# Kernel tuning notes

Hardware: AMD Instinct MI355X
Metric: run time of the kernel (lower is better)

## Reference

```python
import jax, jax.numpy as jnp
import numpy as np

DIM = 768

def setup_inputs() -> dict:
    key = jax.random.key(0)
    ks = jax.random.split(key, 11)
    B, N = 4, 2048
    s = 1.0 / np.sqrt(DIM)
    inp = {
        "q": jax.random.normal(ks[0], (B, N, DIM), jnp.float32),
        "k": jax.random.normal(ks[1], (B, N, DIM), jnp.float32),
        "v": jax.random.normal(ks[2], (B, N, DIM), jnp.float32),
        "Wq": jax.random.normal(ks[3], (DIM, DIM), jnp.float32) * s,
        "bq": jnp.zeros((DIM,), jnp.float32),
        "Wk": jax.random.normal(ks[4], (DIM, DIM), jnp.float32) * s,
        "bk": jnp.zeros((DIM,), jnp.float32),
        "Wv": jax.random.normal(ks[5], (DIM, DIM), jnp.float32) * s,
        "bv": jnp.zeros((DIM,), jnp.float32),
        "Wp": jax.random.normal(ks[6], (DIM, DIM), jnp.float32) * s,
        "bp": jnp.zeros((DIM,), jnp.float32),
    }
    return inp

def reference(q, k, v, Wq, bq, Wk, bk, Wv, bv, Wp, bp):
    # Linear projections (torch Linear: x @ W.T + b)
    scale = DIM ** (-0.5)  # note: full dim, num_heads unused in original forward
    qp = q @ Wq.T + bq            # [B, Nq, D]
    kp = k @ Wk.T + bk            # [B, Nk, D]
    vp = v @ Wv.T + bv            # [B, Nk, D]
    attn = jnp.einsum('bqd,bkd->bqk', qp * scale, kp)  # [B, Nq, Nk]
    attn = jax.nn.softmax(attn, axis=-1)
    x = jnp.einsum('bqk,bkd->bqd', attn, vp)           # [B, Nq, D]
    return x @ Wp.T + bp
```

## Files before the change

### kernel.cpp

```cpp
#include <hip/hip_runtime.h>
#include <hip/hip_bf16.h>
#include <math.h>

typedef __bf16 bf16x8 __attribute__((ext_vector_type(8)));
typedef float  f32x4  __attribute__((ext_vector_type(4)));
typedef float  f32x4v __attribute__((ext_vector_type(4)));
typedef unsigned short ushort_t;
typedef ushort_t u16x4 __attribute__((ext_vector_type(4)));
typedef ushort_t u16x8 __attribute__((ext_vector_type(8)));

__device__ __forceinline__ ushort_t f2bf(float f) {
    unsigned u = __builtin_bit_cast(unsigned, f);
    u += 0x7FFFu + ((u >> 16) & 1u);
    return (ushort_t)(u >> 16);
}
__device__ __forceinline__ float bf2f(ushort_t b) {
    return __builtin_bit_cast(float, (unsigned)b << 16);
}

__device__ __forceinline__ void xcd_remap(int& bx, int& by, int& bz) {
    const int gx = gridDim.x, gy = gridDim.y;
    const int nwg = gx * gy * gridDim.z;
    const int lin = (blockIdx.z * gy + blockIdx.y) * gx + blockIdx.x;
    const int chunk = nwg >> 3;
    int nid = (lin & 7) * chunk + (lin >> 3);
    bx = nid % gx; nid /= gx;
    by = nid % gy; bz = nid / gy;
}

__global__ __launch_bounds__(256)
void cvt_all(const float* __restrict__ v, const float* __restrict__ Wq,
             const float* __restrict__ Wk, const float* __restrict__ Wv,
             const float* __restrict__ Wp,
             ushort_t* __restrict__ vb, ushort_t* __restrict__ Wqb,
             ushort_t* __restrict__ Wkb, ushort_t* __restrict__ Wvb,
             ushort_t* __restrict__ Wpb, float* __restrict__ rowsum)
{
    const int b = blockIdx.x;
    if (b < 6144) {
        int i = b * 256 + threadIdx.x;
        f32x4v x = ((const f32x4v*)v)[i];
        u16x4 o = { f2bf(x.x), f2bf(x.y), f2bf(x.z), f2bf(x.w) };
        ((u16x4*)vb)[i] = o;
    } else if (b < 8448) {
        const int w = (b - 6144) / 576;
        const int bb = (b - 6144) % 576;
        const float* in  = w == 0 ? Wq : w == 1 ? Wk : w == 2 ? Wv : Wp;
        ushort_t*    out = w == 0 ? Wqb : w == 1 ? Wkb : w == 2 ? Wvb : Wpb;
        int i = bb * 256 + threadIdx.x;
        f32x4v x = ((const f32x4v*)in)[i];
        u16x4 o = { f2bf(x.x), f2bf(x.y), f2bf(x.z), f2bf(x.w) };
        ((u16x4*)out)[i] = o;
    } else {
        int i = (b - 8448) * 256 + threadIdx.x;
        rowsum[i] = 0.f;
    }
}

#define GEMM256_CORE(Ab_, lda_, Bb_, ldb_, Kdim_)                                           \
    __shared__ __align__(16) ushort_t lds[2][2][2][128 * 64];                               \
    const int tid  = threadIdx.x;                                                           \
    const int lane = tid & 63;                                                              \
    const int wave = tid >> 6;                                                              \
    const int wm = wave >> 2, wn = wave & 3;                                                \
    const int r16 = lane & 15, kb = lane >> 4;                                              \
    f32x4 acc[8][4];                                                                        \
    _Pragma("unroll") for (int i = 0; i < 8; ++i)                                           \
        _Pragma("unroll") for (int j = 0; j < 4; ++j)                                       \
            acc[i][j] = (f32x4){0.f, 0.f, 0.f, 0.f};                                        \
    auto stage = [&](int kt) {                                                              \
        const int d  = kt & 1;                                                              \
        const int k0 = kt * 64;                                                             \
        _Pragma("unroll") for (int arr = 0; arr < 2; ++arr)                                 \
        _Pragma("unroll") for (int h = 0; h < 2; ++h)                                       \
        _Pragma("unroll") for (int l = 0; l < 2; ++l) {                                     \
            const int idx = l * 512 + tid;                                                  \
            const int row = idx >> 3, sl = idx & 7;                                         \
            const int ssrc = sl ^ (row & 7);                                                \
            const long long grow = h * 128 + row;                                           \
            const ushort_t* g = (arr == 0)                                                  \
                ? (Ab_) + (tM + grow) * (long long)(lda_) + k0 + ssrc * 8                   \
                : (Bb_) + (tN + grow) * (long long)(ldb_) + k0 + ssrc * 8;                  \
            ushort_t* lp = &lds[d][arr][h][idx * 8];                                        \
            __builtin_amdgcn_global_load_lds((const __attribute__((address_space(1))) void*)g, \
                                             (__attribute__((address_space(3))) void*)lp, 16, 0, 0); \
        }                                                                                   \
    };                                                                                      \
    auto compute = [&](int kt) {                                                            \
        const int d = kt & 1;                                                               \
        _Pragma("unroll") for (int kk = 0; kk < 2; ++kk) {                                  \
            bf16x8 bfr[4];                                                                  \
            _Pragma("unroll") for (int ni = 0; ni < 4; ++ni) {                              \
                const int row = (wn & 1) * 64 + ni * 16 + r16;                              \
                const int o16 = row * 8 + ((kk * 4 + kb) ^ (row & 7));                      \
                bfr[ni] = *(const bf16x8*)((const char*)&lds[d][1][wn >> 1][0] + o16 * 16); \
            }                                                                               \
            __builtin_amdgcn_s_setprio(1);                                                  \
            _Pragma("unroll") for (int mi = 0; mi < 8; ++mi) {                              \
                const int row = mi * 16 + r16;                                              \
                const int o16 = row * 8 + ((kk * 4 + kb) ^ (row & 7));                      \
                bf16x8 af = *(const bf16x8*)((const char*)&lds[d][0][wm][0] + o16 * 16);    \
                _Pragma("unroll") for (int ni = 0; ni < 4; ++ni)                            \
                    acc[mi][ni] = __builtin_amdgcn_mfma_f32_16x16x32_bf16(af, bfr[ni], acc[mi][ni], 0, 0, 0); \
            }                                                                               \
            __builtin_amdgcn_s_setprio(0);                                                  \
        }                                                                                   \
    };                                                                                      \
    const int NT = (Kdim_) / 64;                                                            \
    stage(0);                                                                               \
    __syncthreads();                                                                        \
    for (int t = 0; t < NT; ++t) {                                                          \
        if (t + 1 < NT) stage(t + 1);                                                       \
        compute(t);                                                                         \
        __syncthreads();                                                                    \
    }                                                                                       \
    const int rquad = (lane >> 4) * 4;                                                      \
    const int cl    = lane & 15;

__global__ __launch_bounds__(512, 2)
void vprojcvt(const ushort_t* __restrict__ wv_, const ushort_t* __restrict__ vb_,
              const float* __restrict__ bv_, ushort_t* __restrict__ dvT_,
              const float* __restrict__ qf_, const float* __restrict__ kf_,
              ushort_t* __restrict__ qb_, ushort_t* __restrict__ kb_)
{
    if (blockIdx.x < 96) {
        const int id = blockIdx.x;
        const long long tM = (long long)(id % 3) * 256;
        const long long tN = (long long)(id / 3) * 256;
        const ushort_t* Ab = wv_;
        const ushort_t* Bb = vb_;

        GEMM256_CORE(Ab, 768, Bb, 768, 768)

#pragma unroll
        for (int mi = 0; mi < 8; ++mi) {
            const long long r = tM + wm * 128 + mi * 16 + rquad;
#pragma unroll
            for (int ni = 0; ni < 4; ++ni) {
                f32x4 v = acc[mi][ni];
                const long long c = tN + wn * 64 + ni * 16 + cl;
#pragma unroll
                for (int j = 0; j < 4; ++j)
                    dvT_[(r + j) * 8192 + c] = f2bf(v[j] + bv_[r + j]);
            }
        }
    } else {
        const long long stride = 160LL * 512;
        for (long long i = (long long)(blockIdx.x - 96) * 512 + threadIdx.x;
             i < 2LL * 1572864; i += stride) {
            const float* src; ushort_t* dst; long long off;
            if (i < 1572864) { src = qf_; dst = qb_; off = i; }
            else             { src = kf_; dst = kb_; off = i - 1572864; }
            f32x4v v4 = ((const f32x4v*)src)[off];
            u16x4 o = { f2bf(v4.x), f2bf(v4.y), f2bf(v4.z), f2bf(v4.w) };
            ((u16x4*)dst)[off] = o;
        }
    }
}

__global__ __launch_bounds__(512, 2)
void projqk2(const ushort_t* __restrict__ qin, const ushort_t* __restrict__ kin,
             const ushort_t* __restrict__ Wqb, const ushort_t* __restrict__ Wkb,
             const float* __restrict__ bqv, const float* __restrict__ bkv,
             ushort_t* __restrict__ dq, ushort_t* __restrict__ dk)
{
    int bx, by, bz;
    xcd_remap(bx, by, bz);
    const int z = bz;
    const long long tM = (long long)by * 256;
    const long long tN = (long long)bx * 256;
    const ushort_t* Ab = z ? kin : qin;
    const ushort_t* Bb = z ? Wkb : Wqb;
    const float* bias  = z ? bkv : bqv;
    ushort_t* dst      = z ? dk : dq;

    GEMM256_CORE(Ab, 768, Bb, 768, 768)

#pragma unroll
    for (int mi = 0; mi < 8; ++mi) {
        const long long r = tM + wm * 128 + mi * 16 + rquad;
#pragma unroll
        for (int ni = 0; ni < 4; ++ni) {
            f32x4 v = acc[mi][ni];
            const long long c = tN + wn * 64 + ni * 16 + cl;
            const float bc = bias[c];
#pragma unroll
            for (int j = 0; j < 4; ++j)
                dst[(r + j) * 768 + c] = f2bf(v[j] + bc);
        }
    }
}

__global__ __launch_bounds__(512, 2)
void sexp2(const ushort_t* __restrict__ qp, const ushort_t* __restrict__ kp,
           ushort_t* __restrict__ P, float* __restrict__ rowsum, float scale)
{
    int bx, by, bz;
    xcd_remap(bx, by, bz);
    const long long tM = (long long)by * 256;
    const long long tN = (long long)bx * 256;
    const int z = bz;
    const ushort_t* Ab = qp + (long long)z * 1572864;
    const ushort_t* Bb = kp + (long long)z * 1572864;

    GEMM256_CORE(Ab, 768, Bb, 768, 768)

    ushort_t* out = P + (long long)z * 4194304;
#pragma unroll
    for (int mi = 0; mi < 8; ++mi) {
        const long long r = tM + wm * 128 + mi * 16 + rquad;
        float rs[4] = {0.f, 0.f, 0.f, 0.f};
#pragma unroll
        for (int ni = 0; ni < 4; ++ni) {
            f32x4 v = acc[mi][ni];
            const long long c = tN + wn * 64 + ni * 16 + cl;
#pragma unroll
            for (int j = 0; j < 4; ++j) {
                float p = __expf(v[j] * scale);
                ushort_t pb = f2bf(p);
                out[(r + j) * 2048 + c] = pb;
                rs[j] += bf2f(pb);
            }
        }
#pragma unroll
        for (int j = 0; j < 4; ++j) {
            float s = rs[j];
            s += __shfl_xor(s, 1, 64);
            s += __shfl_xor(s, 2, 64);
            s += __shfl_xor(s, 4, 64);
            s += __shfl_xor(s, 8, 64);
            if (cl == 0) atomicAdd(&rowsum[(long long)z * 2048 + r + j], s);
        }
    }
}

#define M_PVN  1
#define M_OUT  2

#define BM 128
#define BN 128
#define BK 32

#define GEMM_CORE(Ab_, lda_, Bb_, ldb_, Kdim_)                                              \
    __shared__ __align__(16) ushort_t lds[2][2][BM * BK];                                   \
    const int tid  = threadIdx.x;                                                           \
    const int lane = tid & 63;                                                              \
    const int wave = tid >> 6;                                                              \
    const int wr = wave >> 1, wc = wave & 1;                                                \
    f32x4 acc[4][4];                                                                        \
    _Pragma("unroll") for (int i = 0; i < 4; ++i)                                           \
        _Pragma("unroll") for (int j = 0; j < 4; ++j)                                       \
            acc[i][j] = (f32x4){0.f, 0.f, 0.f, 0.f};                                        \
    auto stage = [&](int buf, int kt) {                                                     \
        const int k0 = kt * BK;                                                             \
        _Pragma("unroll") for (int rnd = 0; rnd < 2; ++rnd) {                               \
            const int c    = tid + rnd * 256;                                               \
            const int row  = c >> 2;                                                        \
            const int slot = (c & 3) ^ (row & 3);                                           \
            const ushort_t* ga = (Ab_) + (tM + row) * (long long)(lda_) + k0 + slot * 8;    \
            const ushort_t* gb = (Bb_) + (tN + row) * (long long)(ldb_) + k0 + slot * 8;    \
            ushort_t* la = &lds[buf][0][(rnd * 256 + wave * 64) * 8];                       \
            ushort_t* lb = &lds[buf][1][(rnd * 256 + wave * 64) * 8];                       \
            __builtin_amdgcn_global_load_lds((const __attribute__((address_space(1))) void*)ga, \
                                             (__attribute__((address_space(3))) void*)la, 16, 0, 0); \
            __builtin_amdgcn_global_load_lds((const __attribute__((address_space(1))) void*)gb, \
                                             (__attribute__((address_space(3))) void*)lb, 16, 0, 0); \
        }                                                                                   \
    };                                                                                      \
    auto compute = [&](int buf) {                                                           \
        const int kb  = lane >> 4;                                                          \
        const int r16 = lane & 15;                                                          \
        bf16x8 af[4], bfr[4];                                                               \
        _Pragma("unroll") for (int mi = 0; mi < 4; ++mi) {                                  \
            const int row = wr * 64 + mi * 16 + r16;                                        \
            const int off = row * 64 + ((kb ^ (row & 3)) << 4);                             \
            af[mi] = *(const bf16x8*)((const char*)lds[buf][0] + off);                      \
        }                                                                                   \
        _Pragma("unroll") for (int ni = 0; ni < 4; ++ni) {                                  \
            const int row = wc * 64 + ni * 16 + r16;                                        \
            const int off = row * 64 + ((kb ^ (row & 3)) << 4);                             \
            bfr[ni] = *(const bf16x8*)((const char*)lds[buf][1] + off);                     \
        }                                                                                   \
        _Pragma("unroll") for (int mi = 0; mi < 4; ++mi)                                    \
            _Pragma("unroll") for (int ni = 0; ni < 4; ++ni)                                \
                acc[mi][ni] = __builtin_amdgcn_mfma_f32_16x16x32_bf16(af[mi], bfr[ni], acc[mi][ni], 0, 0, 0); \
    };                                                                                      \
    const int NT = (Kdim_) / BK;                                                            \
    stage(0, 0);                                                                            \
    __syncthreads();                                                                        \
    int cur = 0;                                                                            \
    for (int kt = 0; kt + 1 < NT; ++kt) {                                                   \
        stage(cur ^ 1, kt + 1);                                                             \
        compute(cur);                                                                       \
        __syncthreads();                                                                    \
        cur ^= 1;                                                                           \
    }                                                                                       \
    compute(cur);                                                                           \
    const int rquad = (lane >> 4) * 4;                                                      \
    const int cl    = lane & 15;

template<int MODE>
__global__ __launch_bounds__(256, 3)
void gemm_nt(const ushort_t* __restrict__ A, int lda, long long aBatch,
             const ushort_t* __restrict__ B, int ldb, long long bBatch,
             void* __restrict__ Cv, int ldc, long long cBatch,
             const float* __restrict__ bias, float* __restrict__ rowsum,
             int K)
{
    int bx, by, bz;
    xcd_remap(bx, by, bz);
    const long long tM = (long long)by * BM;
    const long long tN = (long long)bx * BN;
    const int z = bz;
    const ushort_t* Ab = A + (long long)z * aBatch;
    const ushort_t* Bb = B + (long long)z * bBatch;

    GEMM_CORE(Ab, lda, Bb, ldb, K)

#pragma unroll
    for (int mi = 0; mi < 4; ++mi) {
        const long long r = tM + wr * 64 + mi * 16 + rquad;
        if constexpr (MODE == M_PVN) {
            ushort_t* out = (ushort_t*)Cv + (long long)z * cBatch;
            float inv[4];
#pragma unroll
            for (int j = 0; j < 4; ++j)
                inv[j] = 1.0f / rowsum[(long long)z * 2048 + r + j];
#pragma unroll
            for (int ni = 0; ni < 4; ++ni) {
                f32x4 v = acc[mi][ni];
                const long long c = tN + wc * 64 + ni * 16 + cl;
#pragma unroll
                for (int j = 0; j < 4; ++j)
                    out[(r + j) * ldc + c] = f2bf(v[j] * inv[j]);
            }
        } else {
            float* out = (float*)Cv;
#pragma unroll
            for (int ni = 0; ni < 4; ++ni) {
                f32x4 v = acc[mi][ni];
                const long long c = tN + wc * 64 + ni * 16 + cl;
                const float bc = bias[c];
#pragma unroll
                for (int j = 0; j < 4; ++j)
                    out[(r + j) * ldc + c] = v[j] + bc;
            }
        }
    }
}

extern "C" void kernel_launch(void* const* d_in, const int* in_sizes, int n_in,
                              void* d_out, int out_size, void* d_ws, size_t ws_size,
                              hipStream_t stream) {
    (void)in_sizes; (void)n_in; (void)out_size; (void)ws_size;
    const float* q  = (const float*)d_in[0];
    const float* k  = (const float*)d_in[1];
    const float* v  = (const float*)d_in[2];
    const float* Wq = (const float*)d_in[3];
    const float* bq = (const float*)d_in[4];
    const float* Wk = (const float*)d_in[5];
    const float* bk = (const float*)d_in[6];
    const float* Wv = (const float*)d_in[7];
    const float* bv = (const float*)d_in[8];
    const float* Wp = (const float*)d_in[9];
    const float* bp = (const float*)d_in[10];
    float* out = (float*)d_out;

    char* ws = (char*)d_ws;
    ushort_t* vb  = (ushort_t*)(ws);
    ushort_t* qb  = (ushort_t*)(ws + 12582912LL);
    ushort_t* kb  = (ushort_t*)(ws + 25165824LL);
    ushort_t* P   = (ushort_t*)(ws + 12582912LL);
    ushort_t* Wqb = (ushort_t*)(ws + 46137344LL);
    ushort_t* Wkb = (ushort_t*)(ws + 47316992LL);
    ushort_t* Wvb = (ushort_t*)(ws + 48496640LL);
    ushort_t* Wpb = (ushort_t*)(ws + 49676288LL);
    ushort_t* qp  = (ushort_t*)(ws + 50855936LL);
    ushort_t* kp  = (ushort_t*)(ws + 63438848LL);
    ushort_t* vpT = (ushort_t*)(ws + 76021760LL);
    float* rowsum = (float*)(ws + 88604672LL);
    ushort_t* Ob  = qp;

    const float scale = 1.0f / sqrtf(768.0f);

    cvt_all<<<8480, 256, 0, stream>>>(v, Wq, Wk, Wv, Wp, vb, Wqb, Wkb, Wvb, Wpb, rowsum);

    vprojcvt<<<256, 512, 0, stream>>>(Wvb, vb, bv, vpT, q, k, qb, kb);

    projqk2<<<dim3(3, 32, 2), 512, 0, stream>>>(qb, kb, Wqb, Wkb, bq, bk, qp, kp);

    sexp2<<<dim3(8, 8, 4), 512, 0, stream>>>(qp, kp, P, rowsum, scale);

    gemm_nt<M_PVN><<<dim3(6, 16, 4), 256, 0, stream>>>(P, 2048, 4194304, vpT, 8192, 2048,
                                                       Ob, 768, 1572864, nullptr, rowsum, 2048);
    gemm_nt<M_OUT><<<dim3(6, 64, 1), 256, 0, stream>>>(Ob, 768, 0, Wpb, 768, 0, out, 768, 0, bp, nullptr, 768);
}
```

Baseline: 157.4 us.

## Compute softmax row sums via MFMA with ones in PV GEMM, drop atomics

Removes the rowsum buffer, its zeroing pass in the conversion kernel, and the shuffle-plus-atomicAdd row reduction in the score/exp kernel. Instead, the PV GEMM issues one extra MFMA per row tile against a vector of bf16 ones, so the denominator comes out of the same P tiles it already loads. The generic templated GEMM is split into two specialised kernels with constant strides. This trades the atomic traffic and reduction work in the exp kernel for roughly a quarter more MFMA work in the PV kernel, and each of its six column blocks recomputes the same row sums.

```diff
diff --git a/kernel.cpp b/kernel.cpp
--- a/kernel.cpp
+++ b/kernel.cpp
@@ -13,9 +13,6 @@
     unsigned u = __builtin_bit_cast(unsigned, f);
     u += 0x7FFFu + ((u >> 16) & 1u);
     return (ushort_t)(u >> 16);
-}
-__device__ __forceinline__ float bf2f(ushort_t b) {
-    return __builtin_bit_cast(float, (unsigned)b << 16);
 }
 
 __device__ __forceinline__ void xcd_remap(int& bx, int& by, int& bz) {
@@ -34,7 +31,7 @@
              const float* __restrict__ Wp,
              ushort_t* __restrict__ vb, ushort_t* __restrict__ Wqb,
              ushort_t* __restrict__ Wkb, ushort_t* __restrict__ Wvb,
-             ushort_t* __restrict__ Wpb, float* __restrict__ rowsum)
+             ushort_t* __restrict__ Wpb)
 {
     const int b = blockIdx.x;
     if (b < 6144) {
@@ -42,7 +39,7 @@
         f32x4v x = ((const f32x4v*)v)[i];
         u16x4 o = { f2bf(x.x), f2bf(x.y), f2bf(x.z), f2bf(x.w) };
         ((u16x4*)vb)[i] = o;
-    } else if (b < 8448) {
+    } else {
         const int w = (b - 6144) / 576;
         const int bb = (b - 6144) % 576;
         const float* in  = w == 0 ? Wq : w == 1 ? Wk : w == 2 ? Wv : Wp;
@@ -51,9 +48,6 @@
         f32x4v x = ((const f32x4v*)in)[i];
         u16x4 o = { f2bf(x.x), f2bf(x.y), f2bf(x.z), f2bf(x.w) };
         ((u16x4*)out)[i] = o;
-    } else {
-        int i = (b - 8448) * 256 + threadIdx.x;
-        rowsum[i] = 0.f;
     }
 }
 
@@ -193,7 +187,7 @@
 
 __global__ __launch_bounds__(512, 2)
 void sexp2(const ushort_t* __restrict__ qp, const ushort_t* __restrict__ kp,
-           ushort_t* __restrict__ P, float* __restrict__ rowsum, float scale)
+           ushort_t* __restrict__ P, float scale)
 {
     int bx, by, bz;
     xcd_remap(bx, by, bz);
@@ -209,142 +203,209 @@
 #pragma unroll
     for (int mi = 0; mi < 8; ++mi) {
         const long long r = tM + wm * 128 + mi * 16 + rquad;
-        float rs[4] = {0.f, 0.f, 0.f, 0.f};
 #pragma unroll
         for (int ni = 0; ni < 4; ++ni) {
             f32x4 v = acc[mi][ni];
             const long long c = tN + wn * 64 + ni * 16 + cl;
 #pragma unroll
-            for (int j = 0; j < 4; ++j) {
-                float p = __expf(v[j] * scale);
-                ushort_t pb = f2bf(p);
-                out[(r + j) * 2048 + c] = pb;
-                rs[j] += bf2f(pb);
-            }
-        }
-#pragma unroll
-        for (int j = 0; j < 4; ++j) {
-            float s = rs[j];
-            s += __shfl_xor(s, 1, 64);
-            s += __shfl_xor(s, 2, 64);
-            s += __shfl_xor(s, 4, 64);
-            s += __shfl_xor(s, 8, 64);
-            if (cl == 0) atomicAdd(&rowsum[(long long)z * 2048 + r + j], s);
-        }
-    }
-}
-
-#define M_PVN  1
-#define M_OUT  2
-
-#define BM 128
-#define BN 128
-#define BK 32
-
-#define GEMM_CORE(Ab_, lda_, Bb_, ldb_, Kdim_)                                              \
-    __shared__ __align__(16) ushort_t lds[2][2][BM * BK];                                   \
-    const int tid  = threadIdx.x;                                                           \
-    const int lane = tid & 63;                                                              \
-    const int wave = tid >> 6;                                                              \
-    const int wr = wave >> 1, wc = wave & 1;                                                \
-    f32x4 acc[4][4];                                                                        \
-    _Pragma("unroll") for (int i = 0; i < 4; ++i)                                           \
-        _Pragma("unroll") for (int j = 0; j < 4; ++j)                                       \
-            acc[i][j] = (f32x4){0.f, 0.f, 0.f, 0.f};                                        \
-    auto stage = [&](int buf, int kt) {                                                     \
-        const int k0 = kt * BK;                                                             \
-        _Pragma("unroll") for (int rnd = 0; rnd < 2; ++rnd) {                               \
-            const int c    = tid + rnd * 256;                                               \
-            const int row  = c >> 2;                                                        \
-            const int slot = (c & 3) ^ (row & 3);                                           \
-            const ushort_t* ga = (Ab_) + (tM + row) * (long long)(lda_) + k0 + slot * 8;    \
-            const ushort_t* gb = (Bb_) + (tN + row) * (long long)(ldb_) + k0 + slot * 8;    \
-            ushort_t* la = &lds[buf][0][(rnd * 256 + wave * 64) * 8];                       \
-            ushort_t* lb = &lds[buf][1][(rnd * 256 + wave * 64) * 8];                       \
-            __builtin_amdgcn_global_load_lds((const __attribute__((address_space(1))) void*)ga, \
-                                             (__attribute__((address_space(3))) void*)la, 16, 0, 0); \
-            __builtin_amdgcn_global_load_lds((const __attribute__((address_space(1))) void*)gb, \
-                                             (__attribute__((address_space(3))) void*)lb, 16, 0, 0); \
-        }                                                                                   \
-    };                                                                                      \
-    auto compute = [&](int buf) {                                                           \
-        const int kb  = lane >> 4;                                                          \
-        const int r16 = lane & 15;                                                          \
-        bf16x8 af[4], bfr[4];                                                               \
-        _Pragma("unroll") for (int mi = 0; mi < 4; ++mi) {                                  \
-            const int row = wr * 64 + mi * 16 + r16;                                        \
-            const int off = row * 64 + ((kb ^ (row & 3)) << 4);                             \
-            af[mi] = *(const bf16x8*)((const char*)lds[buf][0] + off);                      \
-        }                                                                                   \
-        _Pragma("unroll") for (int ni = 0; ni < 4; ++ni) {                                  \
-            const int row = wc * 64 + ni * 16 + r16;                                        \
-            const int off = row * 64 + ((kb ^ (row & 3)) << 4);                             \
-            bfr[ni] = *(const bf16x8*)((const char*)lds[buf][1] + off);                     \
-        }                                                                                   \
-        _Pragma("unroll") for (int mi = 0; mi < 4; ++mi)                                    \
-            _Pragma("unroll") for (int ni = 0; ni < 4; ++ni)                                \
-                acc[mi][ni] = __builtin_amdgcn_mfma_f32_16x16x32_bf16(af[mi], bfr[ni], acc[mi][ni], 0, 0, 0); \
-    };                                                                                      \
-    const int NT = (Kdim_) / BK;                                                            \
-    stage(0, 0);                                                                            \
-    __syncthreads();                                                                        \
-    int cur = 0;                                                                            \
-    for (int kt = 0; kt + 1 < NT; ++kt) {                                                   \
-        stage(cur ^ 1, kt + 1);                                                             \
-        compute(cur);                                                                       \
-        __syncthreads();                                                                    \
-        cur ^= 1;                                                                           \
-    }                                                                                       \
-    compute(cur);                                                                           \
-    const int rquad = (lane >> 4) * 4;                                                      \
-    const int cl    = lane & 15;
-
-template<int MODE>
+            for (int j = 0; j < 4; ++j)
+                out[(r + j) * 2048 + c] = f2bf(__expf(v[j] * scale));
+        }
+    }
+}
+
 __global__ __launch_bounds__(256, 3)
-void gemm_nt(const ushort_t* __restrict__ A, int lda, long long aBatch,
-             const ushort_t* __restrict__ B, int ldb, long long bBatch,
-             void* __restrict__ Cv, int ldc, long long cBatch,
-             const float* __restrict__ bias, float* __restrict__ rowsum,
-             int K)
+void pvn_rs(const ushort_t* __restrict__ Pg, const ushort_t* __restrict__ vpT,
+            ushort_t* __restrict__ Og)
 {
     int bx, by, bz;
     xcd_remap(bx, by, bz);
-    const long long tM = (long long)by * BM;
-    const long long tN = (long long)bx * BN;
+    const long long tM = (long long)by * 128;
+    const long long tN = (long long)bx * 128;
     const int z = bz;
-    const ushort_t* Ab = A + (long long)z * aBatch;
-    const ushort_t* Bb = B + (long long)z * bBatch;
-
-    GEMM_CORE(Ab, lda, Bb, ldb, K)
-
+    const ushort_t* Ab = Pg + (long long)z * 4194304;
+    const ushort_t* Bb = vpT + (long long)z * 2048;
+
+    __shared__ __align__(16) ushort_t lds[2][2][128 * 32];
+    const int tid  = threadIdx.x;
+    const int lane = tid & 63;
+    const int wave = tid >> 6;
+    const int wr = wave >> 1, wc = wave & 1;
+
+    const u16x8 oneb = {0x3F80,0x3F80,0x3F80,0x3F80,0x3F80,0x3F80,0x3F80,0x3F80};
+    const bf16x8 ones = __builtin_bit_cast(bf16x8, oneb);
+
+    f32x4 acc[4][4];
+    f32x4 rs4[4];
+#pragma unroll
+    for (int i = 0; i < 4; ++i) {
+        rs4[i] = (f32x4){0.f, 0.f, 0.f, 0.f};
+#pragma unroll
+        for (int j = 0; j < 4; ++j)
+            acc[i][j] = (f32x4){0.f, 0.f, 0.f, 0.f};
+    }
+
+    auto stage = [&](int buf, int kt) {
+        const int k0 = kt * 32;
+#pragma unroll
+        for (int rnd = 0; rnd < 2; ++rnd) {
+            const int c    = tid + rnd * 256;
+            const int row  = c >> 2;
+            const int slot = (c & 3) ^ (row & 3);
+            const ushort_t* ga = Ab + (tM + row) * 2048LL + k0 + slot * 8;
+            const ushort_t* gb = Bb + (tN + row) * 8192LL + k0 + slot * 8;
+            ushort_t* la = &lds[buf][0][(rnd * 256 + wave * 64) * 8];
+            ushort_t* lb = &lds[buf][1][(rnd * 256 + wave * 64) * 8];
+            __builtin_amdgcn_global_load_lds((const __attribute__((address_space(1))) void*)ga,
+                                             (__attribute__((address_space(3))) void*)la, 16, 0, 0);
+            __builtin_amdgcn_global_load_lds((const __attribute__((address_space(1))) void*)gb,
+                                             (__attribute__((address_space(3))) void*)lb, 16, 0, 0);
+        }
+    };
+    auto compute = [&](int buf) {
+        const int kb  = lane >> 4;
+        const int r16 = lane & 15;
+        bf16x8 af[4], bfr[4];
+#pragma unroll
+        for (int mi = 0; mi < 4; ++mi) {
+            const int row = wr * 64 + mi * 16 + r16;
+            const int off = row * 64 + ((kb ^ (row & 3)) << 4);
+            af[mi] = *(const bf16x8*)((const char*)lds[buf][0] + off);
+        }
+#pragma unroll
+        for (int ni = 0; ni < 4; ++ni) {
+            const int row = wc * 64 + ni * 16 + r16;
+            const int off = row * 64 + ((kb ^ (row & 3)) << 4);
+            bfr[ni] = *(const bf16x8*)((const char*)lds[buf][1] + off);
+        }
+#pragma unroll
+        for (int mi = 0; mi < 4; ++mi) {
+#pragma unroll
+            for (int ni = 0; ni < 4; ++ni)
+                acc[mi][ni] = __builtin_amdgcn_mfma_f32_16x16x32_bf16(af[mi], bfr[ni], acc[mi][ni], 0, 0, 0);
+            rs4[mi] = __builtin_amdgcn_mfma_f32_16x16x32_bf16(af[mi], ones, rs4[mi], 0, 0, 0);
+        }
+    };
+
+    stage(0, 0);
+    __syncthreads();
+    int cur = 0;
+    for (int kt = 0; kt + 1 < 64; ++kt) {
+        stage(cur ^ 1, kt + 1);
+        compute(cur);
+        __syncthreads();
+        cur ^= 1;
+    }
+    compute(cur);
+
+    const int rquad = (lane >> 4) * 4;
+    const int cl    = lane & 15;
+    ushort_t* out = Og + (long long)z * 1572864;
 #pragma unroll
     for (int mi = 0; mi < 4; ++mi) {
         const long long r = tM + wr * 64 + mi * 16 + rquad;
-        if constexpr (MODE == M_PVN) {
-            ushort_t* out = (ushort_t*)Cv + (long long)z * cBatch;
-            float inv[4];
+        float inv[4];
+#pragma unroll
+        for (int j = 0; j < 4; ++j)
+            inv[j] = 1.0f / rs4[mi][j];
+#pragma unroll
+        for (int ni = 0; ni < 4; ++ni) {
+            f32x4 v = acc[mi][ni];
+            const long long c = tN + wc * 64 + ni * 16 + cl;
 #pragma unroll
             for (int j = 0; j < 4; ++j)
-                inv[j] = 1.0f / rowsum[(long long)z * 2048 + r + j];
-#pragma unroll
-            for (int ni = 0; ni < 4; ++ni) {
-                f32x4 v = acc[mi][ni];
-                const long long c = tN + wc * 64 + ni * 16 + cl;
-#pragma unroll
-                for (int j = 0; j < 4; ++j)
-                    out[(r + j) * ldc + c] = f2bf(v[j] * inv[j]);
-            }
-        } else {
-            float* out = (float*)Cv;
-#pragma unroll
-            for (int ni = 0; ni < 4; ++ni) {
-                f32x4 v = acc[mi][ni];
-                const long long c = tN + wc * 64 + ni * 16 + cl;
-                const float bc = bias[c];
-#pragma unroll
-                for (int j = 0; j < 4; ++j)
-                    out[(r + j) * ldc + c] = v[j] + bc;
-            }
+                out[(r + j) * 768 + c] = f2bf(v[j] * inv[j]);
+        }
+    }
+}
+
+__global__ __launch_bounds__(256, 3)
+void gemm_out(const ushort_t* __restrict__ A, const ushort_t* __restrict__ B,
+              float* __restrict__ Cg, const float* __restrict__ bias)
+{
+    int bx, by, bz;
+    xcd_remap(bx, by, bz);
+    const long long tM = (long long)by * 128;
+    const long long tN = (long long)bx * 128;
+    const ushort_t* Ab = A;
+    const ushort_t* Bb = B;
+
+    __shared__ __align__(16) ushort_t lds[2][2][128 * 32];
+    const int tid  = threadIdx.x;
+    const int lane = tid & 63;
+    const int wave = tid >> 6;
+    const int wr = wave >> 1, wc = wave & 1;
+    f32x4 acc[4][4];
+#pragma unroll
+    for (int i = 0; i < 4; ++i)
+#pragma unroll
+        for (int j = 0; j < 4; ++j)
+            acc[i][j] = (f32x4){0.f, 0.f, 0.f, 0.f};
+
+    auto stage = [&](int buf, int kt) {
+        const int k0 = kt * 32;
+#pragma unroll
+        for (int rnd = 0; rnd < 2; ++rnd) {
+            const int c    = tid + rnd * 256;
+            const int row  = c >> 2;
+            const int slot = (c & 3) ^ (row & 3);
+            const ushort_t* ga = Ab + (tM + row) * 768LL + k0 + slot * 8;
+            const ushort_t* gb = Bb + (tN + row) * 768LL + k0 + slot * 8;
+            ushort_t* la = &lds[buf][0][(rnd * 256 + wave * 64) * 8];
+            ushort_t* lb = &lds[buf][1][(rnd * 256 + wave * 64) * 8];
+            __builtin_amdgcn_global_load_lds((const __attribute__((address_space(1))) void*)ga,
+                                             (__attribute__((address_space(3))) void*)la, 16, 0, 0);
+            __builtin_amdgcn_global_load_lds((const __attribute__((address_space(1))) void*)gb,
+                                             (__attribute__((address_space(3))) void*)lb, 16, 0, 0);
+        }
+    };
+    auto compute = [&](int buf) {
+        const int kb  = lane >> 4;
+        const int r16 = lane & 15;
+        bf16x8 af[4], bfr[4];
+#pragma unroll
+        for (int mi = 0; mi < 4; ++mi) {
+            const int row = wr * 64 + mi * 16 + r16;
+            const int off = row * 64 + ((kb ^ (row & 3)) << 4);
+            af[mi] = *(const bf16x8*)((const char*)lds[buf][0] + off);
+        }
+#pragma unroll
+        for (int ni = 0; ni < 4; ++ni) {
+            const int row = wc * 64 + ni * 16 + r16;
+            const int off = row * 64 + ((kb ^ (row & 3)) << 4);
+            bfr[ni] = *(const bf16x8*)((const char*)lds[buf][1] + off);
+        }
+#pragma unroll
+        for (int mi = 0; mi < 4; ++mi)
+#pragma unroll
+            for (int ni = 0; ni < 4; ++ni)
+                acc[mi][ni] = __builtin_amdgcn_mfma_f32_16x16x32_bf16(af[mi], bfr[ni], acc[mi][ni], 0, 0, 0);
+    };
+
+    stage(0, 0);
+    __syncthreads();
+    int cur = 0;
+    for (int kt = 0; kt + 1 < 24; ++kt) {
+        stage(cur ^ 1, kt + 1);
+        compute(cur);
+        __syncthreads();
+        cur ^= 1;
+    }
+    compute(cur);
+
+    const int rquad = (lane >> 4) * 4;
+    const int cl    = lane & 15;
+#pragma unroll
+    for (int mi = 0; mi < 4; ++mi) {
+        const long long r = tM + wr * 64 + mi * 16 + rquad;
+#pragma unroll
+        for (int ni = 0; ni < 4; ++ni) {
+            f32x4 v = acc[mi][ni];
+            const long long c = tN + wc * 64 + ni * 16 + cl;
+            const float bc = bias[c];
+#pragma unroll
+            for (int j = 0; j < 4; ++j)
+                Cg[(r + j) * 768 + c] = v[j] + bc;
         }
     }
 }
@@ -378,20 +439,19 @@
     ushort_t* qp  = (ushort_t*)(ws + 50855936LL);
     ushort_t* kp  = (ushort_t*)(ws + 63438848LL);
     ushort_t* vpT = (ushort_t*)(ws + 76021760LL);
-    float* rowsum = (float*)(ws + 88604672LL);
     ushort_t* Ob  = qp;
 
     const float scale = 1.0f / sqrtf(768.0f);
 
-    cvt_all<<<8480, 256, 0, stream>>>(v, Wq, Wk, Wv, Wp, vb, Wqb, Wkb, Wvb, Wpb, rowsum);
+    cvt_all<<<8448, 256, 0, stream>>>(v, Wq, Wk, Wv, Wp, vb, Wqb, Wkb, Wvb, Wpb);
 
     vprojcvt<<<256, 512, 0, stream>>>(Wvb, vb, bv, vpT, q, k, qb, kb);
 
     projqk2<<<dim3(3, 32, 2), 512, 0, stream>>>(qb, kb, Wqb, Wkb, bq, bk, qp, kp);
 
-    sexp2<<<dim3(8, 8, 4), 512, 0, stream>>>(qp, kp, P, rowsum, scale);
-
-    gemm_nt<M_PVN><<<dim3(6, 16, 4), 256, 0, stream>>>(P, 2048, 4194304, vpT, 8192, 2048,
-                                                       Ob, 768, 1572864, nullptr, rowsum, 2048);
-    gemm_nt<M_OUT><<<dim3(6, 64, 1), 256, 0, stream>>>(Ob, 768, 0, Wpb, 768, 0, out, 768, 0, bp, nullptr, 768);
-}
+    sexp2<<<dim3(8, 8, 4), 512, 0, stream>>>(qp, kp, P, scale);
+
+    pvn_rs<<<dim3(6, 16, 4), 256, 0, stream>>>(P, vpT, Ob);
+
+    gemm_out<<<dim3(6, 64, 1), 256, 0, stream>>>(Ob, Wpb, out, bp);
+}
```

New measurement: 153.1 us. 1.03x faster.
